# Optimization experiments

Hardware: AMD Instinct MI355X
Metric: run time of the kernel (lower is better)

The kernel has to match this reference:

```python
import jax, jax.numpy as jnp
import numpy as np

N_NODES = 100000
N_EDGES = 3200000
D_IN = 128
D_HID = 16
N_CLS = 2


def gcn_conv(x, edge_index, W, b, n_nodes):
    """PyG GCNConv (normalize=True, add_self_loops=True, bias=True)."""
    h = x @ W  # [N, out]
    loop = jnp.arange(n_nodes, dtype=edge_index.dtype)
    src = jnp.concatenate([edge_index[0], loop])
    dst = jnp.concatenate([edge_index[1], loop])
    deg = jax.ops.segment_sum(jnp.ones_like(dst, dtype=h.dtype), dst, num_segments=n_nodes)
    dinv = jnp.where(deg > 0, jax.lax.rsqrt(deg), jnp.zeros_like(deg))
    norm = dinv[src] * dinv[dst]  # [E+N]
    msg = h[src] * norm[:, None]  # gather + scale
    out = jax.ops.segment_sum(msg, dst, num_segments=n_nodes)  # scatter-add
    return out + b


def setup_inputs() -> dict:
    key = jax.random.key(0)
    k1, k2, k3, k4, k5 = jax.random.split(key, 5)
    x = jax.random.normal(k1, (N_NODES, D_IN), dtype=jnp.float32)
    edge_index = jax.random.randint(k2, (2, N_EDGES), 0, N_NODES, dtype=jnp.int64)
    # Glorot-style init for GCNConv weights, zeros for bias (PyG default)
    W1 = jax.random.normal(k3, (D_IN, D_HID), dtype=jnp.float32) * (1.0 / np.sqrt(D_IN))
    b1 = jnp.zeros((D_HID,), dtype=jnp.float32)
    W2 = jax.random.normal(k4, (D_HID, N_CLS), dtype=jnp.float32) * (1.0 / np.sqrt(D_HID))
    b2 = jnp.zeros((N_CLS,), dtype=jnp.float32)
    return {"x": x, "edge_index": edge_index, "W1": W1, "b1": b1, "W2": W2, "b2": b2}


def reference(x, edge_index, W1, b1, W2, b2):
    n = x.shape[0]
    h = gcn_conv(x, edge_index, W1, b1, n)
    h = jax.nn.relu(h)
    # dropout is identity in eval mode
    h = gcn_conv(h, edge_index, W2, b2, n)
    return jax.nn.log_softmax(h, axis=1)
```

## Files before the change

kernel.cpp:

```cpp
#include <hip/hip_runtime.h>
#include <hip/hip_bf16.h>
#include <hip/hip_fp16.h>

#define D_IN  128
#define D_HID 16
#define N_CLS 2
#define NPB   256
#define MAXB  512
#define TILE  4096
#define XROW  136

#define FE 0

typedef short bf16x8 __attribute__((ext_vector_type(8)));
typedef float f32x4  __attribute__((ext_vector_type(4)));

__device__ __forceinline__ unsigned short f2bf(float f) {
    unsigned int u = __float_as_uint(f);
    u += 0x7FFFu + ((u >> 16) & 1u);
    return (unsigned short)(u >> 16);
}

template<bool I64>
__device__ __forceinline__ int lde(const void* p, size_t i) {
    if constexpr (I64) return (int)((const long long*)p)[i];
    else               return ((const int*)p)[i];
}

__global__ void k_detect(const int* __restrict__ ev, int* __restrict__ flags) {
    __shared__ int sE;
    if (threadIdx.x == 0) sE = 0;
    __syncthreads();
    if (ev[2 * threadIdx.x + 1] != 0) atomicOr(&sE, 1);
    __syncthreads();
    if (threadIdx.x == 0) flags[FE] = sE ? 0 : 1;
}

template<bool I64>
__device__ __forceinline__ void part_body(
        const void* __restrict__ ei, unsigned int* __restrict__ gcur,
        unsigned int* __restrict__ staged, int E, int cap,
        unsigned int* sbuf, unsigned short* bbuf,
        int* hist, int* lbase, int* gb, int* wsum) {
    int tid = threadIdx.x;
    int t0 = blockIdx.x * TILE;

    hist[tid] = 0;
    __syncthreads();

    int myB[8]; unsigned int myP[8]; int myR[8];
#pragma unroll
    for (int k = 0; k < 8; ++k) {
        int e = t0 + k * 512 + tid;
        if (e < E) {
            int s = lde<I64>(ei, (size_t)e);
            int d = lde<I64>(ei, (size_t)E + e);
            int b = d >> 8;
            myB[k] = b;
            myP[k] = ((unsigned int)s << 8) | (unsigned int)(d & 255);
            myR[k] = atomicAdd(&hist[b], 1);
        } else myB[k] = -1;
    }
    __syncthreads();

    int v = hist[tid];
    int lane = tid & 63, wv = tid >> 6;
    int s = v;
#pragma unroll
    for (int m = 1; m < 64; m <<= 1) {
        int t = __shfl_up(s, m, 64);
        if (lane >= m) s += t;
    }
    if (lane == 63) wsum[wv] = s;
    __syncthreads();
    int woff = 0;
#pragma unroll
    for (int w = 0; w < 8; ++w) if (w < wv) woff += wsum[w];
    int excl = s + woff - v;
    lbase[tid] = excl;
    int gb_ = 0;
    if (v > 0) gb_ = (int)atomicAdd(&gcur[tid], (unsigned int)v);
    gb[tid] = gb_;
    __syncthreads();

#pragma unroll
    for (int k = 0; k < 8; ++k) {
        if (myB[k] >= 0) {
            int pos = lbase[myB[k]] + myR[k];
            sbuf[pos] = myP[k];
            bbuf[pos] = (unsigned short)myB[k];
        }
    }
    __syncthreads();

    int tot = lbase[MAXB - 1] + hist[MAXB - 1];
    for (int i = tid; i < tot; i += 512) {
        int b = bbuf[i];
        int rel = gb[b] + (i - lbase[b]);
        if (rel < cap)
            staged[(size_t)b * cap + rel] = sbuf[i];
    }
}

__global__ __launch_bounds__(512) void k_part(
        const void* __restrict__ ei, unsigned int* __restrict__ gcur,
        unsigned int* __restrict__ staged, int E, int cap) {
    __shared__ unsigned int sbuf[TILE];
    __shared__ unsigned short bbuf[TILE];
    __shared__ int hist[MAXB], lbase[MAXB], gb[MAXB];
    __shared__ int wsum[8];
    __shared__ int sI64;
    int tid = threadIdx.x;
    if (tid == 0) sI64 = 1;
    __syncthreads();
    if (tid < 256 && 2 * tid + 1 < 2 * E && ((const int*)ei)[2 * tid + 1] != 0) sI64 = 0;
    __syncthreads();
    if (sI64) part_body<true >(ei, gcur, staged, E, cap, sbuf, bbuf, hist, lbase, gb, wsum);
    else      part_body<false>(ei, gcur, staged, E, cap, sbuf, bbuf, hist, lbase, gb, wsum);
}

__global__ __launch_bounds__(512) void k_sortd(
        const unsigned int* __restrict__ staged, const unsigned int* __restrict__ gcur,
        unsigned int* __restrict__ staged2, unsigned int* __restrict__ dmeta,
        float* __restrict__ dinv, int cap, int N) {
    __shared__ unsigned int h[NPB];
    __shared__ unsigned int cur[NPB];
    __shared__ int wsum[4];
    int tid = threadIdx.x, b = blockIdx.x;
    long long s0 = (long long)b * cap;
    int cnt = (int)gcur[b];
    if (cnt > cap - NPB) cnt = cap - NPB;
    if (tid < NPB) h[tid] = 0u;
    __syncthreads();
    for (int i = tid; i < cnt; i += 512)
        atomicAdd(&h[staged[s0 + i] & 255], 1u);
    __syncthreads();
    int v = 0, sIncl = 0;
    int lane = tid & 63, wv = tid >> 6;
    if (tid < NPB) {
        v = (int)h[tid];
        sIncl = v;
#pragma unroll
        for (int m = 1; m < 64; m <<= 1) {
            int t = __shfl_up(sIncl, m, 64);
            if (lane >= m) sIncl += t;
        }
        if (lane == 63) wsum[wv] = sIncl;
    }
    __syncthreads();
    if (tid < NPB) {
        int woff = 0;
#pragma unroll
        for (int w = 0; w < 4; ++w) if (w < wv) woff += wsum[w];
        int excl = sIncl + woff - v;
        int node = b * NPB + tid;
        int start = excl + tid;
        dmeta[node] = ((unsigned int)start << 16) | (unsigned int)v;
        cur[tid] = (unsigned int)start;
        if (node < N) dinv[node] = rsqrtf((float)(v + 1));
    }
    __syncthreads();
    for (int i = tid; i < cnt; i += 512) {
        unsigned int p = staged[s0 + i];
        unsigned int r = atomicAdd(&cur[p & 255], 1u);
        staged2[s0 + r] = p;
    }
    __syncthreads();
    if (tid < NPB) {
        unsigned int pos = cur[tid];
        int node = b * NPB + tid;
        if ((int)pos < cap)
            staged2[s0 + pos] = ((unsigned int)node << 8) | (unsigned int)tid;
    }
}

__global__ __launch_bounds__(256) void k_gemm1m(
        const float* __restrict__ x, const float* __restrict__ W1,
        const float* __restrict__ dinv, __half* __restrict__ g1h, int n) {
    __shared__ short xhi[64 * XROW];
    __shared__ short xlo[64 * XROW];
    __shared__ short whi[16 * XROW];
    __shared__ short wlo[16 * XROW];
    int tid = threadIdx.x;
    int node0 = blockIdx.x * 64;

    for (int i = tid; i < D_IN * D_HID; i += 256) {
        int k = i >> 4, f = i & 15;
        float v = W1[i];
        unsigned short h = f2bf(v);
        float fh = __uint_as_float(((unsigned int)h) << 16);
        whi[f * XROW + k] = (short)h;
        wlo[f * XROW + k] = (short)f2bf(v - fh);
    }
    int limFlat = (n - node0) * D_IN;
#pragma unroll
    for (int it = 0; it < 8; ++it) {
        int flat = it * 1024 + tid * 4;
        float4 v = make_float4(0.f, 0.f, 0.f, 0.f);
        if (flat < limFlat) v = *(const float4*)(x + (size_t)node0 * D_IN + flat);
        int row = flat >> 7, k = flat & 127;
        unsigned short h0 = f2bf(v.x), h1 = f2bf(v.y), h2 = f2bf(v.z), h3 = f2bf(v.w);
        unsigned short l0 = f2bf(v.x - __uint_as_float(((unsigned int)h0) << 16));
        unsigned short l1 = f2bf(v.y - __uint_as_float(((unsigned int)h1) << 16));
        unsigned short l2 = f2bf(v.z - __uint_as_float(((unsigned int)h2) << 16));
        unsigned short l3 = f2bf(v.w - __uint_as_float(((unsigned int)h3) << 16));
        int o = row * XROW + k;
        *(uint2*)(&xhi[o]) = make_uint2((unsigned int)h0 | ((unsigned int)h1 << 16),
                                        (unsigned int)h2 | ((unsigned int)h3 << 16));
        *(uint2*)(&xlo[o]) = make_uint2((unsigned int)l0 | ((unsigned int)l1 << 16),
                                        (unsigned int)l2 | ((unsigned int)l3 << 16));
    }
    __syncthreads();

    int w = tid >> 6, L = tid & 63;
    int m = L & 15, q = L >> 4;
    const short* axh = &xhi[(w * 16 + m) * XROW + q * 8];
    const short* axl = &xlo[(w * 16 + m) * XROW + q * 8];
    const short* bwh = &whi[m * XROW + q * 8];
    const short* bwl = &wlo[m * XROW + q * 8];
    f32x4 acc = {0.f, 0.f, 0.f, 0.f};
#pragma unroll
    for (int c = 0; c < 4; ++c) {
        bf16x8 ah = *(const bf16x8*)(axh + c * 32);
        bf16x8 al = *(const bf16x8*)(axl + c * 32);
        bf16x8 bh = *(const bf16x8*)(bwh + c * 32);
        bf16x8 bl = *(const bf16x8*)(bwl + c * 32);
        acc = __builtin_amdgcn_mfma_f32_16x16x32_bf16(ah, bh, acc, 0, 0, 0);
        acc = __builtin_amdgcn_mfma_f32_16x16x32_bf16(ah, bl, acc, 0, 0, 0);
        acc = __builtin_amdgcn_mfma_f32_16x16x32_bf16(al, bh, acc, 0, 0, 0);
    }
    int nodeB = node0 + w * 16 + q * 4;
#pragma unroll
    for (int r = 0; r < 4; ++r) {
        int node = nodeB + r;
        if (node < n) g1h[(size_t)node * D_HID + m] = __float2half(dinv[node] * acc[r]);
    }
}

__global__ __launch_bounds__(256) void k_agg1w(
        const unsigned int* __restrict__ staged2, const unsigned int* __restrict__ dmeta,
        const __half* __restrict__ g1h,
        const float* __restrict__ b1, const float* __restrict__ W2,
        float2* __restrict__ g2, int N, int cap) {
    int tid = threadIdx.x, b = blockIdx.x, by = blockIdx.y;
    long long s0 = (long long)b * cap;
    int lane = tid & 63;
    int f2 = lane & 7;
    int e8 = lane >> 3;
    int wid = (by << 2) + (tid >> 6);
    const __half2* g1h2 = (const __half2*)g1h;
    int f0 = f2 * 2;
    float b10 = b1[f0], b11 = b1[f0 + 1];
    float w00 = W2[f0 * N_CLS + 0], w01 = W2[f0 * N_CLS + 1];
    float w10 = W2[(f0 + 1) * N_CLS + 0], w11 = W2[(f0 + 1) * N_CLS + 1];
    unsigned int md[8];
#pragma unroll
    for (int k = 0; k < 8; ++k) md[k] = dmeta[b * NPB + wid + (k << 5)];
#pragma unroll 2
    for (int k = 0; k < 8; ++k) {
        int node = b * NPB + wid + (k << 5);
        const unsigned int* sp = staged2 + s0 + (md[k] >> 16);
        int cnt = (int)(md[k] & 0xFFFFu) + 1;
        float ax = 0.f, ay = 0.f;
        for (int base = 0; base < cnt; base += 64) {
            unsigned int pe[8];
#pragma unroll
            for (int j = 0; j < 8; ++j) {
                int idx = base + (j << 3) + e8;
                int c = idx < cnt ? idx : cnt - 1;
                pe[j] = sp[c];
            }
#pragma unroll
            for (int j = 0; j < 8; ++j) {
                int idx = base + (j << 3) + e8;
                float2 t = __half22float2(g1h2[(size_t)(pe[j] >> 8) * 8 + f2]);
                if (idx < cnt) { ax += t.x; ay += t.y; }
            }
        }
        ax += __shfl_xor(ax, 8, 64);  ay += __shfl_xor(ay, 8, 64);
        ax += __shfl_xor(ax, 16, 64); ay += __shfl_xor(ay, 16, 64);
        ax += __shfl_xor(ax, 32, 64); ay += __shfl_xor(ay, 32, 64);
        float di = rsqrtf((float)cnt);
        float r0 = fmaxf(b10 + di * ax, 0.f);
        float r1 = fmaxf(b11 + di * ay, 0.f);
        float c0 = r0 * w00 + r1 * w10;
        float c1 = r0 * w01 + r1 * w11;
        c0 += __shfl_xor(c0, 1, 64); c1 += __shfl_xor(c1, 1, 64);
        c0 += __shfl_xor(c0, 2, 64); c1 += __shfl_xor(c1, 2, 64);
        c0 += __shfl_xor(c0, 4, 64); c1 += __shfl_xor(c1, 4, 64);
        if (lane == 0 && node < N) g2[node] = make_float2(di * c0, di * c1);
    }
}

__global__ __launch_bounds__(256) void k_agg2w(
        const unsigned int* __restrict__ staged2, const unsigned int* __restrict__ dmeta,
        const float2* __restrict__ g2,
        const float* __restrict__ b2, float2* __restrict__ out, int N, int cap) {
    int tid = threadIdx.x, b = blockIdx.x, by = blockIdx.y;
    long long s0 = (long long)b * cap;
    int lane = tid & 63;
    int wid = (by << 2) + (tid >> 6);
    float bb0 = b2[0], bb1 = b2[1];
    unsigned int md[8];
#pragma unroll
    for (int k = 0; k < 8; ++k) md[k] = dmeta[b * NPB + wid + (k << 5)];
#pragma unroll 2
    for (int k = 0; k < 8; ++k) {
        int node = b * NPB + wid + (k << 5);
        const unsigned int* sp = staged2 + s0 + (md[k] >> 16);
        int cnt = (int)(md[k] & 0xFFFFu) + 1;
        float a0 = 0.f, a1 = 0.f;
        for (int base = 0; base < cnt; base += 64) {
            int idx = base + lane;
            int c = idx < cnt ? idx : cnt - 1;
            unsigned int p = sp[c];
            float2 t = g2[p >> 8];
            if (idx < cnt) { a0 += t.x; a1 += t.y; }
        }
#pragma unroll
        for (int mm = 1; mm < 64; mm <<= 1) {
            a0 += __shfl_xor(a0, mm, 64);
            a1 += __shfl_xor(a1, mm, 64);
        }
        if (lane == 0 && node < N) {
            float di = rsqrtf((float)cnt);
            float v0 = bb0 + di * a0;
            float v1 = bb1 + di * a1;
            float mx = fmaxf(v0, v1);
            float lse = mx + logf(expf(v0 - mx) + expf(v1 - mx));
            out[node] = make_float2(v0 - lse, v1 - lse);
        }
    }
}

__global__ void fb_deg_init(unsigned int* __restrict__ deg, int n) {
    int i = blockIdx.x * blockDim.x + threadIdx.x;
    if (i < n) deg[i] = 1u;
}
template<bool I64>
__global__ void fb_deg_count(const void* __restrict__ ei, unsigned int* __restrict__ deg,
                             int E, const int* __restrict__ flags) {
    if (flags[FE] != (int)I64) return;
    int e = blockIdx.x * blockDim.x + threadIdx.x;
    if (e < E) atomicAdd(&deg[lde<I64>(ei, (size_t)E + e)], 1u);
}
__global__ void fb_dinv_inplace(float* __restrict__ dinv, int n) {
    int i = blockIdx.x * blockDim.x + threadIdx.x;
    if (i < n) {
        unsigned int u = ((const unsigned int*)dinv)[i];
        dinv[i] = rsqrtf((float)u);
    }
}
__global__ void fb_a1_init(const float* __restrict__ h1, const float* __restrict__ dinv,
                           const float* __restrict__ b1, float* __restrict__ a1, int n) {
    int tid = blockIdx.x * blockDim.x + threadIdx.x;
    if (tid >= n * D_HID) return;
    int node = tid >> 4, f = tid & 15;
    float di = dinv[node];
    a1[tid] = b1[f] + di * di * h1[tid];
}
template<bool I64>
__global__ void fb_agg1(const void* __restrict__ ei, const float* __restrict__ dinv,
                        const float* __restrict__ h1, float* __restrict__ a1,
                        int E, const int* __restrict__ flags) {
    if (flags[FE] != (int)I64) return;
    int tid = blockIdx.x * blockDim.x + threadIdx.x;
    int e = tid >> 4, f = tid & 15;
    if (e >= E) return;
    int s = lde<I64>(ei, (size_t)e);
    int d = lde<I64>(ei, (size_t)E + e);
    float norm = dinv[s] * dinv[d];
    atomicAdd(&a1[(size_t)d * D_HID + f], h1[(size_t)s * D_HID + f] * norm);
}
__global__ void fb_relu_gemm2(const float* __restrict__ a1, const float* __restrict__ W2,
                              float* __restrict__ h2, int n) {
    int node = blockIdx.x * blockDim.x + threadIdx.x;
    if (node >= n) return;
    float c0 = 0.f, c1 = 0.f;
    const float* row = a1 + (size_t)node * D_HID;
#pragma unroll
    for (int f = 0; f < D_HID; ++f) {
        float r = fmaxf(row[f], 0.f);
        c0 += r * W2[f * N_CLS + 0];
        c1 += r * W2[f * N_CLS + 1];
    }
    h2[(size_t)node * 2 + 0] = c0;
    h2[(size_t)node * 2 + 1] = c1;
}
__global__ void fb_a2_init(const float* __restrict__ h2, const float* __restrict__ dinv,
                           const float* __restrict__ b2, float* __restrict__ a2, int n) {
    int tid = blockIdx.x * blockDim.x + threadIdx.x;
    if (tid >= n * N_CLS) return;
    int node = tid >> 1, c = tid & 1;
    float di = dinv[node];
    a2[tid] = b2[c] + di * di * h2[tid];
}
template<bool I64>
__global__ void fb_agg2(const void* __restrict__ ei, const float* __restrict__ dinv,
                        const float* __restrict__ h2, float* __restrict__ a2,
                        int E, const int* __restrict__ flags) {
    if (flags[FE] != (int)I64) return;
    int e = blockIdx.x * blockDim.x + threadIdx.x;
    if (e >= E) return;
    int s = lde<I64>(ei, (size_t)e);
    int d = lde<I64>(ei, (size_t)E + e);
    float norm = dinv[s] * dinv[d];
    atomicAdd(&a2[(size_t)d * 2 + 0], h2[(size_t)s * 2 + 0] * norm);
    atomicAdd(&a2[(size_t)d * 2 + 1], h2[(size_t)s * 2 + 1] * norm);
}
__global__ void fb_gemm1(const float* __restrict__ x, const float* __restrict__ W1,
                         float* __restrict__ h1, int n) {
    __shared__ float w[D_IN * D_HID];
    for (int i = threadIdx.x; i < D_IN * D_HID; i += blockDim.x) w[i] = W1[i];
    __syncthreads();
    int tid = blockIdx.x * blockDim.x + threadIdx.x;
    int node = tid >> 4, f = tid & 15;
    if (node >= n) return;
    const float4* xr = (const float4*)(x + (size_t)node * D_IN);
    float acc = 0.f;
#pragma unroll
    for (int k4 = 0; k4 < D_IN / 4; ++k4) {
        float4 v = xr[k4];
        int k = k4 * 4;
        acc += v.x * w[(k + 0) * D_HID + f];
        acc += v.y * w[(k + 1) * D_HID + f];
        acc += v.z * w[(k + 2) * D_HID + f];
        acc += v.w * w[(k + 3) * D_HID + f];
    }
    h1[tid] = acc;
}
__global__ void fb_lsm(const float* __restrict__ a2, float* __restrict__ out, int n) {
    int node = blockIdx.x * blockDim.x + threadIdx.x;
    if (node >= n) return;
    float v0 = a2[(size_t)node * 2 + 0];
    float v1 = a2[(size_t)node * 2 + 1];
    float m = fmaxf(v0, v1);
    float lse = m + logf(expf(v0 - m) + expf(v1 - m));
    out[(size_t)node * 2 + 0] = v0 - lse;
    out[(size_t)node * 2 + 1] = v1 - lse;
}

extern "C" void kernel_launch(void* const* d_in, const int* in_sizes, int n_in,
                              void* d_out, int out_size, void* d_ws, size_t ws_size,
                              hipStream_t stream) {
    const float* x  = (const float*)d_in[0];
    const void*  ei = d_in[1];
    const float* W1 = (const float*)d_in[2];
    const float* b1 = (const float*)d_in[3];
    const float* W2 = (const float*)d_in[4];
    const float* b2 = (const float*)d_in[5];

    const int N = in_sizes[0] / D_IN;
    const int E = in_sizes[1] / 2;
    const int nb = (N + NPB - 1) / NPB;

    int cap = ((2 * (E / nb + 1) + NPB) + 255) & ~255;
    if (cap < 1024) cap = 1024;

    const int B = 256;
    dim3 blk(B);
    const int nBlkN = (N + B - 1) / B;
    const int nBlkE = (E + B - 1) / B;
    char* ws = (char*)d_ws;

    auto al = [](size_t v) { return (v + 255) & ~(size_t)255; };
    const size_t oDinv   = 0;
    const size_t oDmeta  = al(oDinv + (size_t)N * 4);
    const size_t oGcur   = al(oDmeta + (size_t)nb * NPB * 4);
    const size_t oFlag   = al(oGcur + (size_t)MAXB * 4);
    const size_t oStage  = al(oFlag + 8);
    const size_t oStage2 = al(oStage + (size_t)nb * cap * 4);
    const size_t oG1h    = al(oStage2 + (size_t)nb * cap * 4);
    const size_t oG2     = al(oG1h + (size_t)N * D_HID * 2);
    const size_t needNew = al(oG2 + (size_t)N * 2 * 4);

    if (ws_size >= needNew && nb <= MAXB && cap <= 65280 && N < (1 << 24) - NPB) {
        float*        dinv    = (float*)(ws + oDinv);
        unsigned int* dmeta   = (unsigned int*)(ws + oDmeta);
        unsigned int* gcur    = (unsigned int*)(ws + oGcur);
        unsigned int* staged  = (unsigned int*)(ws + oStage);
        unsigned int* staged2 = (unsigned int*)(ws + oStage2);
        __half*       g1h     = (__half*)(ws + oG1h);
        float2*       g2      = (float2*)(ws + oG2);

        hipMemsetAsync(gcur, 0, (size_t)nb * 4, stream);

        dim3 gPart((E + TILE - 1) / TILE);
        k_part<<<gPart, dim3(512), 0, stream>>>(ei, gcur, staged, E, cap);

        k_sortd<<<dim3(nb), dim3(512), 0, stream>>>(staged, gcur, staged2, dmeta, dinv, cap, N);

        k_gemm1m<<<dim3((N + 63) / 64), dim3(256), 0, stream>>>(x, W1, dinv, g1h, N);

        k_agg1w<<<dim3(nb, 8), dim3(256), 0, stream>>>(staged2, dmeta, g1h, b1, W2, g2, N, cap);

        k_agg2w<<<dim3(nb, 8), dim3(256), 0, stream>>>(staged2, dmeta, g2, b2,
                                                       (float2*)d_out, N, cap);
    } else {
        float* dinv  = (float*)(ws + 0);
        float* h1    = (float*)(ws + 400128);
        float* a1    = (float*)(ws + 6800256);
        float* h2    = (float*)(ws + 13200384);
        float* a2    = (float*)(ws + 14000512);
        int*   flags = (int*)  (ws + 14800640);

        k_detect<<<dim3(1), blk, 0, stream>>>((const int*)ei, flags);
        fb_deg_init<<<dim3(nBlkN), blk, 0, stream>>>((unsigned int*)dinv, N);
        fb_deg_count<false><<<dim3(nBlkE), blk, 0, stream>>>(ei, (unsigned int*)dinv, E, flags);
        fb_deg_count<true ><<<dim3(nBlkE), blk, 0, stream>>>(ei, (unsigned int*)dinv, E, flags);
        fb_dinv_inplace<<<dim3(nBlkN), blk, 0, stream>>>(dinv, N);

        dim3 g_nh((N * D_HID + B - 1) / B);
        fb_gemm1<<<g_nh, blk, 0, stream>>>(x, W1, h1, N);
        fb_a1_init<<<g_nh, blk, 0, stream>>>(h1, dinv, b1, a1, N);
        dim3 g_eh(((size_t)E * D_HID + B - 1) / B);
        fb_agg1<false><<<g_eh, blk, 0, stream>>>(ei, dinv, h1, a1, E, flags);
        fb_agg1<true ><<<g_eh, blk, 0, stream>>>(ei, dinv, h1, a1, E, flags);
        fb_relu_gemm2<<<dim3(nBlkN), blk, 0, stream>>>(a1, W2, h2, N);
        dim3 g_n2((N * N_CLS + B - 1) / B);
        fb_a2_init<<<g_n2, blk, 0, stream>>>(h2, dinv, b2, a2, N);
        fb_agg2<false><<<dim3(nBlkE), blk, 0, stream>>>(ei, dinv, h2, a2, E, flags);
        fb_agg2<true ><<<dim3(nBlkE), blk, 0, stream>>>(ei, dinv, h2, a2, E, flags);
        fb_lsm<<<dim3(nBlkN), blk, 0, stream>>>(a2, (float*)d_out, N);
    }
}
```

Baseline: 222.1 us.

## Fuse sort and both aggregations into one persistent kernel with grid barrier

Degree counting moves into the partition kernel through global atomics, so the GEMM can compute dinv itself without waiting for the sort. The per-bucket sort and both aggregation layers are merged into one persistent kernel that keeps sorted edges in LDS and separates the layers with a software grid barrier. This is meant to remove two kernel launches and the staged2 round trip through global memory. In exchange it adds 3.2M global atomics in k_part, only 391 blocks of 512 threads to do the aggregation work, and a spin-wait barrier that relies on every block being co-resident.

```diff
diff --git a/kernel.cpp b/kernel.cpp
--- a/kernel.cpp
+++ b/kernel.cpp
@@ -9,6 +9,7 @@
 #define MAXB  512
 #define TILE  4096
 #define XROW  136
+#define LCAP  10496
 
 #define FE 0
 
@@ -39,7 +40,8 @@
 template<bool I64>
 __device__ __forceinline__ void part_body(
         const void* __restrict__ ei, unsigned int* __restrict__ gcur,
-        unsigned int* __restrict__ staged, int E, int cap,
+        unsigned int* __restrict__ staged, unsigned int* __restrict__ deg,
+        int E, int cap,
         unsigned int* sbuf, unsigned short* bbuf,
         int* hist, int* lbase, int* gb, int* wsum) {
     int tid = threadIdx.x;
@@ -59,6 +61,7 @@
             myB[k] = b;
             myP[k] = ((unsigned int)s << 8) | (unsigned int)(d & 255);
             myR[k] = atomicAdd(&hist[b], 1);
+            atomicAdd(&deg[d], 1u);
         } else myB[k] = -1;
     }
     __syncthreads();
@@ -104,7 +107,8 @@
 
 __global__ __launch_bounds__(512) void k_part(
         const void* __restrict__ ei, unsigned int* __restrict__ gcur,
-        unsigned int* __restrict__ staged, int E, int cap) {
+        unsigned int* __restrict__ staged, unsigned int* __restrict__ deg,
+        int E, int cap) {
     __shared__ unsigned int sbuf[TILE];
     __shared__ unsigned short bbuf[TILE];
     __shared__ int hist[MAXB], lbase[MAXB], gb[MAXB];
@@ -115,68 +119,13 @@
     __syncthreads();
     if (tid < 256 && 2 * tid + 1 < 2 * E && ((const int*)ei)[2 * tid + 1] != 0) sI64 = 0;
     __syncthreads();
-    if (sI64) part_body<true >(ei, gcur, staged, E, cap, sbuf, bbuf, hist, lbase, gb, wsum);
-    else      part_body<false>(ei, gcur, staged, E, cap, sbuf, bbuf, hist, lbase, gb, wsum);
-}
-
-__global__ __launch_bounds__(512) void k_sortd(
-        const unsigned int* __restrict__ staged, const unsigned int* __restrict__ gcur,
-        unsigned int* __restrict__ staged2, unsigned int* __restrict__ dmeta,
-        float* __restrict__ dinv, int cap, int N) {
-    __shared__ unsigned int h[NPB];
-    __shared__ unsigned int cur[NPB];
-    __shared__ int wsum[4];
-    int tid = threadIdx.x, b = blockIdx.x;
-    long long s0 = (long long)b * cap;
-    int cnt = (int)gcur[b];
-    if (cnt > cap - NPB) cnt = cap - NPB;
-    if (tid < NPB) h[tid] = 0u;
-    __syncthreads();
-    for (int i = tid; i < cnt; i += 512)
-        atomicAdd(&h[staged[s0 + i] & 255], 1u);
-    __syncthreads();
-    int v = 0, sIncl = 0;
-    int lane = tid & 63, wv = tid >> 6;
-    if (tid < NPB) {
-        v = (int)h[tid];
-        sIncl = v;
-#pragma unroll
-        for (int m = 1; m < 64; m <<= 1) {
-            int t = __shfl_up(sIncl, m, 64);
-            if (lane >= m) sIncl += t;
-        }
-        if (lane == 63) wsum[wv] = sIncl;
-    }
-    __syncthreads();
-    if (tid < NPB) {
-        int woff = 0;
-#pragma unroll
-        for (int w = 0; w < 4; ++w) if (w < wv) woff += wsum[w];
-        int excl = sIncl + woff - v;
-        int node = b * NPB + tid;
-        int start = excl + tid;
-        dmeta[node] = ((unsigned int)start << 16) | (unsigned int)v;
-        cur[tid] = (unsigned int)start;
-        if (node < N) dinv[node] = rsqrtf((float)(v + 1));
-    }
-    __syncthreads();
-    for (int i = tid; i < cnt; i += 512) {
-        unsigned int p = staged[s0 + i];
-        unsigned int r = atomicAdd(&cur[p & 255], 1u);
-        staged2[s0 + r] = p;
-    }
-    __syncthreads();
-    if (tid < NPB) {
-        unsigned int pos = cur[tid];
-        int node = b * NPB + tid;
-        if ((int)pos < cap)
-            staged2[s0 + pos] = ((unsigned int)node << 8) | (unsigned int)tid;
-    }
+    if (sI64) part_body<true >(ei, gcur, staged, deg, E, cap, sbuf, bbuf, hist, lbase, gb, wsum);
+    else      part_body<false>(ei, gcur, staged, deg, E, cap, sbuf, bbuf, hist, lbase, gb, wsum);
 }
 
 __global__ __launch_bounds__(256) void k_gemm1m(
         const float* __restrict__ x, const float* __restrict__ W1,
-        const float* __restrict__ dinv, __half* __restrict__ g1h, int n) {
+        const unsigned int* __restrict__ deg, __half* __restrict__ g1h, int n) {
     __shared__ short xhi[64 * XROW];
     __shared__ short xlo[64 * XROW];
     __shared__ short whi[16 * XROW];
@@ -233,7 +182,220 @@
 #pragma unroll
     for (int r = 0; r < 4; ++r) {
         int node = nodeB + r;
-        if (node < n) g1h[(size_t)node * D_HID + m] = __float2half(dinv[node] * acc[r]);
+        if (node < n) {
+            float di = rsqrtf((float)(deg[node] + 1u));
+            g1h[(size_t)node * D_HID + m] = __float2half(di * acc[r]);
+        }
+    }
+}
+
+__device__ __forceinline__ void gbar(unsigned int* bar, int nblk) {
+    __syncthreads();
+    if (threadIdx.x == 0) {
+        __threadfence();
+        __hip_atomic_fetch_add(bar, 1u, __ATOMIC_ACQ_REL, __HIP_MEMORY_SCOPE_AGENT);
+        while (__hip_atomic_load(bar, __ATOMIC_ACQUIRE, __HIP_MEMORY_SCOPE_AGENT)
+               < (unsigned int)nblk)
+            __builtin_amdgcn_s_sleep(2);
+        __threadfence();
+    }
+    __syncthreads();
+}
+
+__global__ __launch_bounds__(512, 4) void k_fuse(
+        const unsigned int* __restrict__ staged, const unsigned int* __restrict__ gcur,
+        unsigned int* __restrict__ staged2,
+        const __half* __restrict__ g1h,
+        const float* __restrict__ b1, const float* __restrict__ W2,
+        const float* __restrict__ b2,
+        float2* __restrict__ g2, float2* __restrict__ out,
+        unsigned int* __restrict__ bar, int nblk, int N, int cap) {
+    __shared__ unsigned int ebuf[LCAP];
+    __shared__ unsigned int md[NPB];
+    __shared__ unsigned int cur[NPB];
+    __shared__ int wsum[4];
+    int tid = threadIdx.x, b = blockIdx.x;
+    long long s0 = (long long)b * cap;
+    int cnt = (int)gcur[b];
+    if (cnt > cap - NPB) cnt = cap - NPB;
+    bool inLds = (cnt + NPB) <= LCAP;
+
+    if (tid < NPB) cur[tid] = 0u;
+    __syncthreads();
+    for (int i = tid; i < cnt; i += 512)
+        atomicAdd(&cur[staged[s0 + i] & 255], 1u);
+    __syncthreads();
+    int lane = tid & 63, wv = tid >> 6;
+    int v = 0, sIncl = 0;
+    if (tid < NPB) {
+        v = (int)cur[tid];
+        sIncl = v;
+#pragma unroll
+        for (int m = 1; m < 64; m <<= 1) {
+            int t = __shfl_up(sIncl, m, 64);
+            if (lane >= m) sIncl += t;
+        }
+        if (lane == 63) wsum[wv] = sIncl;
+    }
+    __syncthreads();
+    if (tid < NPB) {
+        int woff = 0;
+#pragma unroll
+        for (int w = 0; w < 4; ++w) if (w < wv) woff += wsum[w];
+        int start = (sIncl + woff - v) + tid;
+        md[tid] = ((unsigned int)start << 16) | (unsigned int)v;
+        cur[tid] = (unsigned int)start;
+    }
+    __syncthreads();
+    if (inLds) {
+        for (int i = tid; i < cnt; i += 512) {
+            unsigned int p = staged[s0 + i];
+            ebuf[atomicAdd(&cur[p & 255], 1u)] = p;
+        }
+    } else {
+        for (int i = tid; i < cnt; i += 512) {
+            unsigned int p = staged[s0 + i];
+            staged2[s0 + atomicAdd(&cur[p & 255], 1u)] = p;
+        }
+    }
+    __syncthreads();
+    if (tid < NPB) {
+        unsigned int pos = cur[tid];
+        unsigned int sv = ((unsigned int)(b * NPB + tid) << 8) | (unsigned int)tid;
+        if (inLds) ebuf[pos] = sv;
+        else if ((int)pos < cap) staged2[s0 + pos] = sv;
+    }
+    __syncthreads();
+
+    const __half2* g1h2 = (const __half2*)g1h;
+    int f2 = lane & 7, e8 = lane >> 3;
+    int f0 = f2 * 2;
+    float b10 = b1[f0], b11 = b1[f0 + 1];
+    float w00 = W2[f0 * N_CLS + 0], w01 = W2[f0 * N_CLS + 1];
+    float w10 = W2[(f0 + 1) * N_CLS + 0], w11 = W2[(f0 + 1) * N_CLS + 1];
+#pragma unroll 2
+    for (int k = 0; k < 32; ++k) {
+        int dl = wv + (k << 3);
+        unsigned int m = md[dl];
+        int st = (int)(m >> 16);
+        int dcnt = (int)(m & 0xFFFFu) + 1;
+        float ax = 0.f, ay = 0.f;
+        for (int base = 0; base < dcnt; base += 64) {
+            unsigned int pe[8];
+#pragma unroll
+            for (int j = 0; j < 8; ++j) {
+                int idx = base + (j << 3) + e8;
+                int c = idx < dcnt ? idx : dcnt - 1;
+                pe[j] = inLds ? ebuf[st + c] : staged2[s0 + st + c];
+            }
+#pragma unroll
+            for (int j = 0; j < 8; ++j) {
+                int idx = base + (j << 3) + e8;
+                float2 t = __half22float2(g1h2[(size_t)(pe[j] >> 8) * 8 + f2]);
+                if (idx < dcnt) { ax += t.x; ay += t.y; }
+            }
+        }
+        ax += __shfl_xor(ax, 8, 64);  ay += __shfl_xor(ay, 8, 64);
+        ax += __shfl_xor(ax, 16, 64); ay += __shfl_xor(ay, 16, 64);
+        ax += __shfl_xor(ax, 32, 64); ay += __shfl_xor(ay, 32, 64);
+        float di = rsqrtf((float)dcnt);
+        float r0 = fmaxf(b10 + di * ax, 0.f);
+        float r1 = fmaxf(b11 + di * ay, 0.f);
+        float c0 = r0 * w00 + r1 * w10;
+        float c1 = r0 * w01 + r1 * w11;
+        c0 += __shfl_xor(c0, 1, 64); c1 += __shfl_xor(c1, 1, 64);
+        c0 += __shfl_xor(c0, 2, 64); c1 += __shfl_xor(c1, 2, 64);
+        c0 += __shfl_xor(c0, 4, 64); c1 += __shfl_xor(c1, 4, 64);
+        int node = b * NPB + dl;
+        if (lane == 0 && node < N) g2[node] = make_float2(di * c0, di * c1);
+    }
+
+    gbar(bar, nblk);
+
+    float bb0 = b2[0], bb1 = b2[1];
+#pragma unroll 2
+    for (int k = 0; k < 32; ++k) {
+        int dl = wv + (k << 3);
+        unsigned int m = md[dl];
+        int st = (int)(m >> 16);
+        int dcnt = (int)(m & 0xFFFFu) + 1;
+        float a0 = 0.f, a1 = 0.f;
+        for (int base = 0; base < dcnt; base += 64) {
+            int idx = base + lane;
+            int c = idx < dcnt ? idx : dcnt - 1;
+            unsigned int p = inLds ? ebuf[st + c] : staged2[s0 + st + c];
+            float2 t = g2[p >> 8];
+            if (idx < dcnt) { a0 += t.x; a1 += t.y; }
+        }
+#pragma unroll
+        for (int mm = 1; mm < 64; mm <<= 1) {
+            a0 += __shfl_xor(a0, mm, 64);
+            a1 += __shfl_xor(a1, mm, 64);
+        }
+        int node = b * NPB + dl;
+        if (lane == 0 && node < N) {
+            float di = rsqrtf((float)dcnt);
+            float v0 = bb0 + di * a0;
+            float v1 = bb1 + di * a1;
+            float mx = fmaxf(v0, v1);
+            float lse = mx + logf(expf(v0 - mx) + expf(v1 - mx));
+            out[node] = make_float2(v0 - lse, v1 - lse);
+        }
+    }
+}
+
+__global__ __launch_bounds__(512) void k_sortd(
+        const unsigned int* __restrict__ staged, const unsigned int* __restrict__ gcur,
+        unsigned int* __restrict__ staged2, unsigned int* __restrict__ dmeta,
+        float* __restrict__ dinv, int cap, int N) {
+    __shared__ unsigned int h[NPB];
+    __shared__ unsigned int cur[NPB];
+    __shared__ int wsum[4];
+    int tid = threadIdx.x, b = blockIdx.x;
+    long long s0 = (long long)b * cap;
+    int cnt = (int)gcur[b];
+    if (cnt > cap - NPB) cnt = cap - NPB;
+    if (tid < NPB) h[tid] = 0u;
+    __syncthreads();
+    for (int i = tid; i < cnt; i += 512)
+        atomicAdd(&h[staged[s0 + i] & 255], 1u);
+    __syncthreads();
+    int v = 0, sIncl = 0;
+    int lane = tid & 63, wv = tid >> 6;
+    if (tid < NPB) {
+        v = (int)h[tid];
+        sIncl = v;
+#pragma unroll
+        for (int m = 1; m < 64; m <<= 1) {
+            int t = __shfl_up(sIncl, m, 64);
+            if (lane >= m) sIncl += t;
+        }
+        if (lane == 63) wsum[wv] = sIncl;
+    }
+    __syncthreads();
+    if (tid < NPB) {
+        int woff = 0;
+#pragma unroll
+        for (int w = 0; w < 4; ++w) if (w < wv) woff += wsum[w];
+        int excl = sIncl + woff - v;
+        int node = b * NPB + tid;
+        int start = excl + tid;
+        dmeta[node] = ((unsigned int)start << 16) | (unsigned int)v;
+        cur[tid] = (unsigned int)start;
+        if (node < N) dinv[node] = rsqrtf((float)(v + 1));
+    }
+    __syncthreads();
+    for (int i = tid; i < cnt; i += 512) {
+        unsigned int p = staged[s0 + i];
+        unsigned int r = atomicAdd(&cur[p & 255], 1u);
+        staged2[s0 + r] = p;
+    }
+    __syncthreads();
+    if (tid < NPB) {
+        unsigned int pos = cur[tid];
+        int node = b * NPB + tid;
+        if ((int)pos < cap)
+            staged2[s0 + pos] = ((unsigned int)node << 8) | (unsigned int)tid;
     }
 }
 
@@ -453,6 +615,7 @@
     const int N = in_sizes[0] / D_IN;
     const int E = in_sizes[1] / 2;
     const int nb = (N + NPB - 1) / NPB;
+    const int nP = nb * NPB;
 
     int cap = ((2 * (E / nb + 1) + NPB) + 255) & ~255;
     if (cap < 1024) cap = 1024;
@@ -464,38 +627,62 @@
     char* ws = (char*)d_ws;
 
     auto al = [](size_t v) { return (v + 255) & ~(size_t)255; };
-    const size_t oDinv   = 0;
+    const size_t oDeg    = 0;
+    const size_t oGcur   = al(oDeg + (size_t)N * 4);
+    const size_t oBar    = oGcur + (size_t)MAXB * 4;
+    const size_t zeroLen = al(oBar + 256);
+    const size_t oDinv   = zeroLen;
     const size_t oDmeta  = al(oDinv + (size_t)N * 4);
-    const size_t oGcur   = al(oDmeta + (size_t)nb * NPB * 4);
-    const size_t oFlag   = al(oGcur + (size_t)MAXB * 4);
-    const size_t oStage  = al(oFlag + 8);
+    const size_t oStage  = al(oDmeta + (size_t)nP * 4);
     const size_t oStage2 = al(oStage + (size_t)nb * cap * 4);
     const size_t oG1h    = al(oStage2 + (size_t)nb * cap * 4);
-    const size_t oG2     = al(oG1h + (size_t)N * D_HID * 2);
-    const size_t needNew = al(oG2 + (size_t)N * 2 * 4);
+    const size_t oG2     = al(oG1h + (size_t)nP * D_HID * 2);
+    const size_t needNew = al(oG2 + (size_t)nP * 8);
 
     if (ws_size >= needNew && nb <= MAXB && cap <= 65280 && N < (1 << 24) - NPB) {
+        unsigned int* deg     = (unsigned int*)(ws + oDeg);
+        unsigned int* gcur    = (unsigned int*)(ws + oGcur);
+        unsigned int* bar     = (unsigned int*)(ws + oBar);
         float*        dinv    = (float*)(ws + oDinv);
         unsigned int* dmeta   = (unsigned int*)(ws + oDmeta);
-        unsigned int* gcur    = (unsigned int*)(ws + oGcur);
         unsigned int* staged  = (unsigned int*)(ws + oStage);
         unsigned int* staged2 = (unsigned int*)(ws + oStage2);
         __half*       g1h     = (__half*)(ws + oG1h);
         float2*       g2      = (float2*)(ws + oG2);
 
-        hipMemsetAsync(gcur, 0, (size_t)nb * 4, stream);
+        static int s_cu = 0, s_maxB = -1;
+        if (s_maxB < 0) {
+            hipDeviceProp_t prop{};
+            int dev = 0;
+            (void)hipGetDevice(&dev);
+            if (hipGetDeviceProperties(&prop, dev) == hipSuccess)
+                s_cu = prop.multiProcessorCount;
+            int mb = 0;
+            if (hipOccupancyMaxActiveBlocksPerMultiprocessor(&mb, k_fuse, 512, 0) == hipSuccess)
+                s_maxB = mb;
+            else s_maxB = 0;
+        }
+        bool coop = (s_maxB > 0) && ((long long)s_maxB * s_cu >= nb);
+
+        hipMemsetAsync(ws, 0, zeroLen, stream);
 
         dim3 gPart((E + TILE - 1) / TILE);
-        k_part<<<gPart, dim3(512), 0, stream>>>(ei, gcur, staged, E, cap);
-
-        k_sortd<<<dim3(nb), dim3(512), 0, stream>>>(staged, gcur, staged2, dmeta, dinv, cap, N);
-
-        k_gemm1m<<<dim3((N + 63) / 64), dim3(256), 0, stream>>>(x, W1, dinv, g1h, N);
-
-        k_agg1w<<<dim3(nb, 8), dim3(256), 0, stream>>>(staged2, dmeta, g1h, b1, W2, g2, N, cap);
-
-        k_agg2w<<<dim3(nb, 8), dim3(256), 0, stream>>>(staged2, dmeta, g2, b2,
-                                                       (float2*)d_out, N, cap);
+        k_part<<<gPart, dim3(512), 0, stream>>>(ei, gcur, staged, deg, E, cap);
+
+        k_gemm1m<<<dim3((N + 63) / 64), dim3(256), 0, stream>>>(x, W1, deg, g1h, N);
+
+        if (coop) {
+            k_fuse<<<dim3(nb), dim3(512), 0, stream>>>(
+                staged, gcur, staged2, g1h, b1, W2, b2, g2,
+                (float2*)d_out, bar, nb, N, cap);
+        } else {
+            k_sortd<<<dim3(nb), dim3(512), 0, stream>>>(staged, gcur, staged2, dmeta,
+                                                        dinv, cap, N);
+            k_agg1w<<<dim3(nb, 8), dim3(256), 0, stream>>>(staged2, dmeta, g1h, b1, W2,
+                                                           g2, N, cap);
+            k_agg2w<<<dim3(nb, 8), dim3(256), 0, stream>>>(staged2, dmeta, g2, b2,
+                                                           (float2*)d_out, N, cap);
+        }
     } else {
         float* dinv  = (float*)(ws + 0);
         float* h1    = (float*)(ws + 400128);
```

After: 465.1 us. 109% more time.
